# Optimization experiments

Measured on AMD Instinct MI355X. Metric: run time of the kernel, lower is better.

Reference implementation:

```python
import jax, jax.numpy as jnp
import numpy as np

K = 3
PAD = 1


def conv3x3(x, w):
    # x: [B,C,H,W], w: [O,C,3,3] -> [B,O,H,W], stride 1, pad 1, no bias
    return jax.lax.conv_general_dilated(
        x, w, window_strides=(1, 1), padding=((PAD, PAD), (PAD, PAD)),
        dimension_numbers=("NCHW", "OIHW", "NCHW"))


def bilinear_gather(x, py, px):
    """Zero-padded bilinear sampling (torchvision deform_conv2d semantics).
    x: [B,C,H,W]; py, px: [B,KK,H,W] absolute sampling coords.
    Returns [B,C,KK,H,W]."""
    B, C, H, W = x.shape
    KK = py.shape[1]
    y0 = jnp.floor(py)
    x0 = jnp.floor(px)
    wy1 = py - y0  # frac weights
    wx1 = px - x0
    wy0 = 1.0 - wy1
    wx0 = 1.0 - wx1
    x_flat = x.reshape(B, C, H * W)

    def corner(yi, xi, w):
        valid = (yi >= 0) & (yi <= H - 1) & (xi >= 0) & (xi <= W - 1)
        yc = jnp.clip(yi, 0, H - 1).astype(jnp.int32)
        xc = jnp.clip(xi, 0, W - 1).astype(jnp.int32)
        idx = (yc * W + xc).reshape(B, 1, KK * H * W)
        v = jnp.take_along_axis(x_flat, jnp.broadcast_to(idx, (B, C, KK * H * W)), axis=2)
        v = v.reshape(B, C, KK, H, W)
        return v * (w * valid.astype(x.dtype))[:, None]

    return (corner(y0, x0, wy0 * wx0) + corner(y0, x0 + 1.0, wy0 * wx1)
            + corner(y0 + 1.0, x0, wy1 * wx0) + corner(y0 + 1.0, x0 + 1.0, wy1 * wx1))


def deform_conv2d(x, offset, weight):
    """x: [B,C,H,W]; offset: [B,2*K*K,H,W] (dy,dx interleaved per tap, row-major);
    weight: [O,C,K,K]. stride 1, pad 1, dilation 1, 1 group, 1 offset group."""
    B, C, H, W = x.shape
    O = weight.shape[0]
    off = offset.reshape(B, K * K, 2, H, W)
    dy, dx = off[:, :, 0], off[:, :, 1]  # [B,9,H,W]
    ki, kj = jnp.meshgrid(jnp.arange(K, dtype=x.dtype), jnp.arange(K, dtype=x.dtype), indexing="ij")
    ki = ki.reshape(1, K * K, 1, 1)
    kj = kj.reshape(1, K * K, 1, 1)
    hh = jnp.arange(H, dtype=x.dtype).reshape(1, 1, H, 1)
    ww = jnp.arange(W, dtype=x.dtype).reshape(1, 1, 1, W)
    py = hh - PAD + ki + dy  # [B,9,H,W]
    px = ww - PAD + kj + dx
    sampled = bilinear_gather(x, py, px)  # [B,C,9,H,W]
    return jnp.einsum("bckhw,ock->bohw", sampled, weight.reshape(O, C, K * K))


def offset_estimator(x, w1, w2, w3):
    # channel-preserving bottleneck stand-in for Dynamic_offset_estimator
    h = jax.nn.relu(conv3x3(x, w1))
    h = jax.nn.relu(conv3x3(h, w2))
    return conv3x3(h, w3)


def setup_inputs() -> dict:
    key = jax.random.key(0)
    ks = jax.random.split(key, 7)
    B, C, H, W = 1, 768, 64, 64
    C2, CM = 2 * C, 192
    f32 = jnp.float32
    inp = {
        "input_features": jax.random.normal(ks[0], (B, C, H, W), dtype=f32),
        "reference_features": jax.random.normal(ks[1], (B, C, H, W), dtype=f32),
        "est_w1": jax.random.normal(ks[2], (CM, C2, K, K), dtype=f32) / np.sqrt(C2 * K * K),
        "est_w2": jax.random.normal(ks[3], (CM, CM, K, K), dtype=f32) / np.sqrt(CM * K * K),
        "est_w3": jax.random.normal(ks[4], (C2, CM, K, K), dtype=f32) / np.sqrt(CM * K * K),
        "offset_w": jax.random.normal(ks[5], (18, C2, K, K), dtype=f32) / np.sqrt(C2 * K * K),
        "deform_w": jax.random.normal(ks[6], (C, C, K, K), dtype=f32) / np.sqrt(C * K * K),
    }
    return inp


def reference(input_features, reference_features, est_w1, est_w2, est_w3, offset_w, deform_w):
    input_offset = jnp.concatenate([input_features, reference_features], axis=1)  # [B,2C,H,W]
    est = offset_estimator(input_offset, est_w1, est_w2, est_w3)  # [B,2C,H,W]
    offset = conv3x3(est, offset_w)  # [B,18,H,W]
    return deform_conv2d(reference_features, offset, deform_w)  # [B,C,H,W]
```

## Files before the change

kernel.cpp:

```cpp
#include <hip/hip_runtime.h>

#define HWPX 4096

typedef short s8v  __attribute__((ext_vector_type(8)));
typedef float f4v  __attribute__((ext_vector_type(4)));

__device__ inline unsigned short f2bf(float f) {
    unsigned u = __float_as_uint(f);
    return (unsigned short)((u + 0x7fffu + ((u >> 16) & 1u)) >> 16);
}
__device__ inline float bf2f(unsigned s) {
    return __uint_as_float(s << 16);
}

#define GLDS16(gsrc, ldst) \
    __builtin_amdgcn_global_load_lds( \
        (const __attribute__((address_space(1))) unsigned int*)(gsrc), \
        (__attribute__((address_space(3))) unsigned int*)(ldst), 16, 0, 0)

__global__ __launch_bounds__(256)
void tr_cat_k(const float* __restrict__ xa, const float* __restrict__ xb,
              short* __restrict__ xt)
{
    __shared__ __align__(16) short T[64 * 72];
    const int c0 = blockIdx.x * 64, p0 = blockIdx.y * 64, tid = threadIdx.x;
    for (int i = tid; i < 4096; i += 256) {
        int cl = i >> 6, pl = i & 63;
        int c = c0 + cl;
        float v = (c < 768) ? xa[(size_t)c * HWPX + p0 + pl]
                            : xb[(size_t)(c - 768) * HWPX + p0 + pl];
        T[pl * 72 + cl] = (short)f2bf(v);
    }
    __syncthreads();
    for (int i = tid; i < 512; i += 256) {
        int pl = i >> 3, part = i & 7;
        uint4 v = *(const uint4*)&T[pl * 72 + part * 8];
        *(uint4*)&xt[(size_t)(p0 + pl) * 1536 + c0 + part * 8] = v;
    }
}

__device__ inline void wpack1(const float* __restrict__ src, short* __restrict__ dst,
                              int i, int Cin, int Cout, int S, int NB)
{
    int e = i & 7, lane = (i >> 3) & 63;
    int lm = lane & 15, quad = lane >> 4;
    int rest = i >> 9;
    int f = rest % NB;
    int s = (rest / NB) % S;
    int g = rest / (NB * S);
    int cout = g * (NB * 16) + f * 16 + lm;
    int cb = s / 9, t = s % 9;
    int ch = cb * 32 + quad * 8 + e;
    dst[i] = (cout < Cout) ? (short)f2bf(src[((size_t)cout * Cin + ch) * 9 + t]) : 0;
}

#define C1 2654208
#define C2 2985984
#define C3 5640192
#define C4 6082560
#define C5 11390976

__global__ __launch_bounds__(256)
void wpack_all_k(const float* __restrict__ s1, const float* __restrict__ s2,
                 const float* __restrict__ s3, const float* __restrict__ s4,
                 const float* __restrict__ s5,
                 short* __restrict__ d1, short* __restrict__ d2,
                 short* __restrict__ d3, short* __restrict__ d4,
                 short* __restrict__ d5)
{
    int i = blockIdx.x * 256 + threadIdx.x;
    if (i < C1)      wpack1(s1, d1, i,      1536, 192,  432, 4);
    else if (i < C2) wpack1(s2, d2, i - C1, 192,  192,  54,  2);
    else if (i < C3) wpack1(s3, d3, i - C2, 192,  1536, 54,  4);
    else if (i < C4) wpack1(s4, d4, i - C3, 1536, 18,   432, 2);
    else if (i < C5) wpack1(s5, d5, i - C4, 768,  768,  216, 4);
}

template<int NB>
__global__ __launch_bounds__(256, 3)
void convf_k(const short* __restrict__ Xt, int CinStr,
             const short* __restrict__ Wp, int S, int chunks,
             short* __restrict__ Out, int Cstr, int splitStride)
{
    __shared__ __align__(16) short sH[6 * 66 * 40];
    const int tid = threadIdx.x, lane = tid & 63, wv = tid >> 6;
    const int lm = lane & 15, quad = lane >> 4;
    const int r0 = blockIdx.x * 4;
    const int g  = blockIdx.y;
    const int cb0 = blockIdx.z * chunks;
    short* out = Out + (size_t)blockIdx.z * splitStride;

    f4v acc[4][NB];
#pragma unroll
    for (int ma = 0; ma < 4; ++ma)
#pragma unroll
        for (int nb = 0; nb < NB; ++nb)
#pragma unroll
            for (int r = 0; r < 4; ++r) acc[ma][nb][r] = 0.f;

    for (int cc = 0; cc < chunks; ++cc) {
        const int cb = cb0 + cc;
        const short* wpB = Wp + ((size_t)(g * S + cb * 9) * NB) * 512 + lane * 8;
        s8v bb[NB];
#pragma unroll
        for (int f = 0; f < NB; ++f)
            bb[f] = *(const s8v*)&wpB[(size_t)f * 512];

        for (int i = tid; i < 1584; i += 256) {
            int slot = i >> 2, part = i & 3;
            int hr = slot / 66, px = slot % 66;
            int gy = r0 - 1 + hr, gx = px - 1;
            uint4 v = {0, 0, 0, 0};
            if (gy >= 0 && gy < 64 && gx >= 0 && gx < 64)
                v = *(const uint4*)&Xt[(size_t)(gy * 64 + gx) * CinStr + cb * 32 + part * 8];
            *(uint4*)&sH[slot * 40 + part * 8] = v;
        }
        __syncthreads();

#pragma unroll
        for (int t = 0; t < 9; ++t) {
            const int ty = t / 3, tx = t % 3;
            s8v nxt[NB];
#pragma unroll
            for (int f = 0; f < NB; ++f)
                nxt[f] = *(const s8v*)&wpB[(size_t)((t + 1) * NB + f) * 512];
            s8v a[4];
#pragma unroll
            for (int ma = 0; ma < 4; ++ma)
                a[ma] = *(const s8v*)&sH[((wv + ty) * 66 + ma * 16 + lm + tx) * 40 + quad * 8];
#pragma unroll
            for (int ma = 0; ma < 4; ++ma)
#pragma unroll
                for (int nb = 0; nb < NB; ++nb)
                    acc[ma][nb] = __builtin_amdgcn_mfma_f32_16x16x32_bf16(
                        a[ma], bb[nb], acc[ma][nb], 0, 0, 0);
#pragma unroll
            for (int f = 0; f < NB; ++f) bb[f] = nxt[f];
        }
        __syncthreads();
    }

    const int py = (r0 + wv) * 64;
#pragma unroll
    for (int ma = 0; ma < 4; ++ma)
#pragma unroll
        for (int nb = 0; nb < NB; ++nb)
#pragma unroll
            for (int r = 0; r < 4; ++r)
                out[(size_t)(py + ma * 16 + quad * 4 + r) * Cstr
                    + g * (NB * 16) + nb * 16 + lm] = (short)f2bf(acc[ma][nb][r]);
}

__global__ __launch_bounds__(256)
void ep_sumb_k(const short* __restrict__ P, short* __restrict__ outb,
               int nsplit, size_t splitStride, int n8, int relu)
{
    int i = blockIdx.x * 256 + threadIdx.x;
    if (i >= n8) return;
    size_t base = (size_t)i * 8;
    float s[8];
#pragma unroll
    for (int j = 0; j < 8; ++j) s[j] = 0.f;
    for (int sp = 0; sp < nsplit; ++sp) {
        uint4 v = *(const uint4*)&P[sp * splitStride + base];
        s[0] += bf2f(v.x & 0xffffu); s[1] += bf2f(v.x >> 16);
        s[2] += bf2f(v.y & 0xffffu); s[3] += bf2f(v.y >> 16);
        s[4] += bf2f(v.z & 0xffffu); s[5] += bf2f(v.z >> 16);
        s[6] += bf2f(v.w & 0xffffu); s[7] += bf2f(v.w >> 16);
    }
    if (relu) {
#pragma unroll
        for (int j = 0; j < 8; ++j) s[j] = fmaxf(s[j], 0.f);
    }
    uint4 o;
    o.x = f2bf(s[0]) | ((unsigned)f2bf(s[1]) << 16);
    o.y = f2bf(s[2]) | ((unsigned)f2bf(s[3]) << 16);
    o.z = f2bf(s[4]) | ((unsigned)f2bf(s[5]) << 16);
    o.w = f2bf(s[6]) | ((unsigned)f2bf(s[7]) << 16);
    *(uint4*)&outb[base] = o;
}

__global__ __launch_bounds__(256)
void ep_offs_k(const short* __restrict__ P, float* __restrict__ offs, int nsplit)
{
    int i = blockIdx.x * 256 + threadIdx.x;
    if (i >= 18 * HWPX) return;
    int m = i >> 12, px = i & 4095;
    float s = 0.f;
    for (int sp = 0; sp < nsplit; ++sp)
        s += bf2f((unsigned short)P[((size_t)sp * HWPX + px) * 32 + m]);
    offs[i] = s;
}

__global__ __launch_bounds__(256)
void sample_k(const short* __restrict__ xcat, const float* __restrict__ offs,
              short* __restrict__ Smp)
{
    __shared__ int   s_mi[9][16][4];
    __shared__ float s_mw[9][16][4];
    const int tid = threadIdx.x;
    const int p0  = blockIdx.x * 16;
    const int cbq = blockIdx.y * 6;
    const int wv  = tid >> 6, lane = tid & 63;
    const int lmx = lane & 15, qd = lane >> 4;
    const int pg  = p0 >> 6, ma = (p0 >> 4) & 3;

    if (tid < 144) {
        int t = tid / 16, p = tid % 16;
        int pxg = p0 + p;
        int r = pxg >> 6, x = pxg & 63;
        float dy = offs[(size_t)(2 * t)     * HWPX + pxg];
        float dx = offs[(size_t)(2 * t + 1) * HWPX + pxg];
        float py  = (float)(r - 1 + t / 3) + dy;
        float pxf = (float)(x - 1 + t % 3) + dx;
        py  = fminf(fmaxf(py,  -1e6f), 1e6f);
        pxf = fminf(fmaxf(pxf, -1e6f), 1e6f);
        float y0f = floorf(py), x0f = floorf(pxf);
        float wy1 = py - y0f, wx1 = pxf - x0f;
        float wy0 = 1.f - wy1, wx0 = 1.f - wx1;
        bool vy0 = (y0f >=  0.f) && (y0f <= 63.f);
        bool vy1 = (y0f >= -1.f) && (y0f <= 62.f);
        bool vx0 = (x0f >=  0.f) && (x0f <= 63.f);
        bool vx1 = (x0f >= -1.f) && (x0f <= 62.f);
        int y0 = (int)fminf(fmaxf(y0f,       0.f), 63.f);
        int y1 = (int)fminf(fmaxf(y0f + 1.f, 0.f), 63.f);
        int x0 = (int)fminf(fmaxf(x0f,       0.f), 63.f);
        int x1 = (int)fminf(fmaxf(x0f + 1.f, 0.f), 63.f);
        s_mi[t][p][0] = y0 * 64 + x0;  s_mw[t][p][0] = (vy0 && vx0) ? wy0 * wx0 : 0.f;
        s_mi[t][p][1] = y0 * 64 + x1;  s_mw[t][p][1] = (vy0 && vx1) ? wy0 * wx1 : 0.f;
        s_mi[t][p][2] = y1 * 64 + x0;  s_mw[t][p][2] = (vy1 && vx0) ? wy1 * wx0 : 0.f;
        s_mi[t][p][3] = y1 * 64 + x1;  s_mw[t][p][3] = (vy1 && vx1) ? wy1 * wx1 : 0.f;
    }
    __syncthreads();

    for (int j = wv; j < 54; j += 4) {
        const int t = j / 6, cb = cbq + j % 6;
        int   mi[4];
        float mw[4];
#pragma unroll
        for (int c = 0; c < 4; ++c) {
            mi[c] = s_mi[t][lmx][c];
            mw[c] = s_mw[t][lmx][c];
        }
        float a[8];
#pragma unroll
        for (int k = 0; k < 8; ++k) a[k] = 0.f;
#pragma unroll
        for (int c = 0; c < 4; ++c) {
            float wgt = mw[c];
            const short* src = xcat + (size_t)mi[c] * 1536 + 768 + cb * 32 + qd * 8;
            uint4 v = *(const uint4*)src;
            a[0] += wgt * bf2f(v.x & 0xffffu); a[1] += wgt * bf2f(v.x >> 16);
            a[2] += wgt * bf2f(v.y & 0xffffu); a[3] += wgt * bf2f(v.y >> 16);
            a[4] += wgt * bf2f(v.z & 0xffffu); a[5] += wgt * bf2f(v.z >> 16);
            a[6] += wgt * bf2f(v.w & 0xffffu); a[7] += wgt * bf2f(v.w >> 16);
        }
        uint4 o;
        o.x = f2bf(a[0]) | ((unsigned)f2bf(a[1]) << 16);
        o.y = f2bf(a[2]) | ((unsigned)f2bf(a[3]) << 16);
        o.z = f2bf(a[4]) | ((unsigned)f2bf(a[5]) << 16);
        o.w = f2bf(a[6]) | ((unsigned)f2bf(a[7]) << 16);
        size_t addr = ((((size_t)pg * 216 + cb * 9 + t) * 4 + ma) * 64 + lane) * 8;
        *(uint4*)&Smp[addr] = o;
    }
}

__global__ __launch_bounds__(256, 3)
void dgemm_k(const short* __restrict__ Ap, const short* __restrict__ Bp,
             short* __restrict__ P)
{
    __shared__ __align__(16) short sL[3 * 8192];

    const int tid = threadIdx.x, lane = tid & 63, wv = tid >> 6;
    const int lm = lane & 15, quad = lane >> 4;
    const int mg = blockIdx.y * 2 + (wv >> 1);
    const int pg = blockIdx.x * 2 + (wv & 1);
    const int s0 = blockIdx.z * 54;

    const short* stSrc;
    int stChunk;
    if (wv < 2) {
        stSrc = Ap + ((size_t)(blockIdx.y * 2 + wv) * 216 + s0) * 2048;
        stChunk = wv * 2048;
    } else {
        stSrc = Bp + ((size_t)(blockIdx.x * 2 + (wv - 2)) * 216 + s0) * 2048;
        stChunk = 4096 + (wv - 2) * 2048;
    }

    f4v acc[4][4];
#pragma unroll
    for (int ma = 0; ma < 4; ++ma)
#pragma unroll
        for (int nb = 0; nb < 4; ++nb)
#pragma unroll
            for (int r = 0; r < 4; ++r) acc[ma][nb][r] = 0.f;

#pragma unroll
    for (int j = 0; j < 4; ++j)
        GLDS16(stSrc + (size_t)0 * 2048 + j * 512 + lane * 8,
               &sL[0 * 8192 + stChunk + j * 512]);
#pragma unroll
    for (int j = 0; j < 4; ++j)
        GLDS16(stSrc + (size_t)1 * 2048 + j * 512 + lane * 8,
               &sL[1 * 8192 + stChunk + j * 512]);
    asm volatile("s_waitcnt vmcnt(4)" ::: "memory");
    __builtin_amdgcn_s_barrier();
    __builtin_amdgcn_sched_barrier(0);

    const int aOff = (wv >> 1) * 2048;
    const int bOff = 4096 + (wv & 1) * 2048;

    s8v avA[4], bvA[4], avB[4], bvB[4];
#pragma unroll
    for (int f = 0; f < 4; ++f) {
        avA[f] = *(const s8v*)&sL[0 * 8192 + aOff + f * 512 + lane * 8];
        bvA[f] = *(const s8v*)&sL[0 * 8192 + bOff + f * 512 + lane * 8];
    }

    int cA = 0, cB = 1, cC = 2;

    for (int s = 0; s < 52; s += 2) {
#pragma unroll
        for (int j = 0; j < 4; ++j)
            GLDS16(stSrc + (size_t)(s + 2) * 2048 + j * 512 + lane * 8,
                   &sL[cC * 8192 + stChunk + j * 512]);
        asm volatile("s_waitcnt vmcnt(4)" ::: "memory");
        __builtin_amdgcn_s_barrier();
        __builtin_amdgcn_sched_barrier(0);
        {
            const int base = cB * 8192;
#pragma unroll
            for (int f = 0; f < 4; ++f) {
                avB[f] = *(const s8v*)&sL[base + aOff + f * 512 + lane * 8];
                bvB[f] = *(const s8v*)&sL[base + bOff + f * 512 + lane * 8];
            }
        }
#pragma unroll
        for (int ma = 0; ma < 4; ++ma)
#pragma unroll
            for (int nb = 0; nb < 4; ++nb)
                acc[ma][nb] = __builtin_amdgcn_mfma_f32_16x16x32_bf16(
                    avA[ma], bvA[nb], acc[ma][nb], 0, 0, 0);

#pragma unroll
        for (int j = 0; j < 4; ++j)
            GLDS16(stSrc + (size_t)(s + 3) * 2048 + j * 512 + lane * 8,
                   &sL[cA * 8192 + stChunk + j * 512]);
        asm volatile("s_waitcnt vmcnt(4)" ::: "memory");
        __builtin_amdgcn_s_barrier();
        __builtin_amdgcn_sched_barrier(0);
        {
            const int base = cC * 8192;
#pragma unroll
            for (int f = 0; f < 4; ++f) {
                avA[f] = *(const s8v*)&sL[base + aOff + f * 512 + lane * 8];
                bvA[f] = *(const s8v*)&sL[base + bOff + f * 512 + lane * 8];
            }
        }
#pragma unroll
        for (int ma = 0; ma < 4; ++ma)
#pragma unroll
            for (int nb = 0; nb < 4; ++nb)
                acc[ma][nb] = __builtin_amdgcn_mfma_f32_16x16x32_bf16(
                    avB[ma], bvB[nb], acc[ma][nb], 0, 0, 0);

        int nA = cC, nB = cA, nC = cB;
        cA = nA; cB = nB; cC = nC;
    }

    asm volatile("s_waitcnt vmcnt(0)" ::: "memory");
    __builtin_amdgcn_s_barrier();
    __builtin_amdgcn_sched_barrier(0);
    {
        const int base = cB * 8192;
#pragma unroll
        for (int f = 0; f < 4; ++f) {
            avB[f] = *(const s8v*)&sL[base + aOff + f * 512 + lane * 8];
            bvB[f] = *(const s8v*)&sL[base + bOff + f * 512 + lane * 8];
        }
    }
#pragma unroll
    for (int ma = 0; ma < 4; ++ma)
#pragma unroll
        for (int nb = 0; nb < 4; ++nb)
            acc[ma][nb] = __builtin_amdgcn_mfma_f32_16x16x32_bf16(
                avA[ma], bvA[nb], acc[ma][nb], 0, 0, 0);
#pragma unroll
    for (int ma = 0; ma < 4; ++ma)
#pragma unroll
        for (int nb = 0; nb < 4; ++nb)
            acc[ma][nb] = __builtin_amdgcn_mfma_f32_16x16x32_bf16(
                avB[ma], bvB[nb], acc[ma][nb], 0, 0, 0);

    short* p = P + (size_t)blockIdx.z * 768 * HWPX;
#pragma unroll
    for (int ma = 0; ma < 4; ++ma)
#pragma unroll
        for (int nb = 0; nb < 4; ++nb)
#pragma unroll
            for (int r = 0; r < 4; ++r)
                p[(size_t)(mg * 64 + ma * 16 + quad * 4 + r) * HWPX
                  + pg * 64 + nb * 16 + lm] = (short)f2bf(acc[ma][nb][r]);
}

__global__ __launch_bounds__(256)
void ep_dg_k(const short* __restrict__ P, float* __restrict__ out)
{
    int i = blockIdx.x * 256 + threadIdx.x;
    if (i >= 768 * HWPX / 8) return;
    size_t base = (size_t)i * 8;
    float s[8];
#pragma unroll
    for (int j = 0; j < 8; ++j) s[j] = 0.f;
    for (int sp = 0; sp < 4; ++sp) {
        uint4 v = *(const uint4*)&P[(size_t)sp * 768 * HWPX + base];
        s[0] += bf2f(v.x & 0xffffu); s[1] += bf2f(v.x >> 16);
        s[2] += bf2f(v.y & 0xffffu); s[3] += bf2f(v.y >> 16);
        s[4] += bf2f(v.z & 0xffffu); s[5] += bf2f(v.z >> 16);
        s[6] += bf2f(v.w & 0xffffu); s[7] += bf2f(v.w >> 16);
    }
    float4 o0 = make_float4(s[0], s[1], s[2], s[3]);
    float4 o1 = make_float4(s[4], s[5], s[6], s[7]);
    *(float4*)&out[base]     = o0;
    *(float4*)&out[base + 4] = o1;
}

extern "C" void kernel_launch(void* const* d_in, const int* in_sizes, int n_in,
                              void* d_out, int out_size, void* d_ws, size_t ws_size,
                              hipStream_t stream)
{
    const float* x_in  = (const float*)d_in[0];
    const float* x_ref = (const float*)d_in[1];
    const float* w1    = (const float*)d_in[2];
    const float* w2    = (const float*)d_in[3];
    const float* w3    = (const float*)d_in[4];
    const float* ow    = (const float*)d_in[5];
    const float* dw    = (const float*)d_in[6];
    float* out = (float*)d_out;

    char* w = (char*)d_ws;
    size_t off = 0;
    auto carve = [&](size_t bytes) {
        void* p = w + off;
        off += (bytes + 255) & ~(size_t)255;
        return p;
    };
    short* xcat = (short*)carve((size_t)4096 * 1536 * 2);
    short* w1p  = (short*)carve((size_t)C1 * 2);
    short* w2p  = (short*)carve((size_t)(C2 - C1) * 2);
    short* w3p  = (short*)carve((size_t)(C3 - C2) * 2);
    short* w4p  = (short*)carve((size_t)(C4 - C3) * 2);
    short* dwp  = (short*)carve((size_t)(C5 - C4) * 2);
    float* offs = (float*)carve((size_t)18 * 4096 * 4);
    short* Smp  = (short*)carve((size_t)4096 * 6912 * 2);
    char*  R    = (char*)carve((size_t)2 * 768 * 4096 * 4);
    short* rh1  = (short*)R;
    short* rh2  = (short*)(R + 1572864);
    short* est  = (short*)(R + 3145728);
    short* Pcv  = Smp;
    short* Pdg  = (short*)R;

    tr_cat_k<<<dim3(24, 64), 256, 0, stream>>>(x_in, x_ref, xcat);
    wpack_all_k<<<(C5 + 255) / 256, 256, 0, stream>>>(w1, w2, w3, ow, dw,
                                                      w1p, w2p, w3p, w4p, dwp);

    const int n8 = 4096 * 192 / 8;
    convf_k<4><<<dim3(16, 3, 16), 256, 0, stream>>>(xcat, 1536, w1p, 432, 3,
                                                    Pcv, 192, 4096 * 192);
    ep_sumb_k<<<(n8 + 255) / 256, 256, 0, stream>>>(Pcv, rh1, 16, (size_t)4096 * 192, n8, 1);
    convf_k<2><<<dim3(16, 6, 6), 256, 0, stream>>>(rh1, 192, w2p, 54, 1,
                                                   Pcv, 192, 4096 * 192);
    ep_sumb_k<<<(n8 + 255) / 256, 256, 0, stream>>>(Pcv, rh2, 6, (size_t)4096 * 192, n8, 1);
    convf_k<4><<<dim3(16, 24, 2), 256, 0, stream>>>(rh2, 192, w3p, 54, 3,
                                                    Pcv, 1536, 4096 * 1536);
    {
        const int n8c3 = 4096 * 1536 / 8;
        ep_sumb_k<<<(n8c3 + 255) / 256, 256, 0, stream>>>(Pcv, est, 2, (size_t)4096 * 1536, n8c3, 0);
    }
    convf_k<2><<<dim3(16, 1, 48), 256, 0, stream>>>(est, 1536, w4p, 432, 1,
                                                    Pcv, 32, 4096 * 32);
    ep_offs_k<<<(18 * HWPX + 255) / 256, 256, 0, stream>>>(Pcv, offs, 48);
    sample_k<<<dim3(256, 4), 256, 0, stream>>>(xcat, offs, Smp);
    dgemm_k<<<dim3(32, 6, 4), 256, 0, stream>>>(dwp, Smp, Pdg);
    ep_dg_k<<<(768 * HWPX / 8 + 255) / 256, 256, 0, stream>>>(Pdg, out);
}
```

Baseline: 329.8 us.

## Fuse split-K partial sum into offset conv loads and merge prep kernels

The two split-K partial outputs of the third estimator conv are now summed on the fly while the fourth conv loads its input tile, so the separate ep_sumb reduction kernel and the round trip through the est buffer go away. The transpose/concat kernel and the weight-pack kernel are merged into one launch that picks its role from the block index. The cost is that the offset conv now reads two bf16 buffers and redoes the add-and-round for every halo load, and each value is loaded about three times because of halo overlap. Offset partials now go to a separate p4 buffer so they do not overwrite the Pcv inputs that are still being read.

```diff
diff --git a/kernel.cpp b/kernel.cpp
--- a/kernel.cpp
+++ b/kernel.cpp
@@ -18,26 +18,11 @@
         (const __attribute__((address_space(1))) unsigned int*)(gsrc), \
         (__attribute__((address_space(3))) unsigned int*)(ldst), 16, 0, 0)
 
-__global__ __launch_bounds__(256)
-void tr_cat_k(const float* __restrict__ xa, const float* __restrict__ xb,
-              short* __restrict__ xt)
-{
-    __shared__ __align__(16) short T[64 * 72];
-    const int c0 = blockIdx.x * 64, p0 = blockIdx.y * 64, tid = threadIdx.x;
-    for (int i = tid; i < 4096; i += 256) {
-        int cl = i >> 6, pl = i & 63;
-        int c = c0 + cl;
-        float v = (c < 768) ? xa[(size_t)c * HWPX + p0 + pl]
-                            : xb[(size_t)(c - 768) * HWPX + p0 + pl];
-        T[pl * 72 + cl] = (short)f2bf(v);
-    }
-    __syncthreads();
-    for (int i = tid; i < 512; i += 256) {
-        int pl = i >> 3, part = i & 7;
-        uint4 v = *(const uint4*)&T[pl * 72 + part * 8];
-        *(uint4*)&xt[(size_t)(p0 + pl) * 1536 + c0 + part * 8] = v;
-    }
-}
+#define C1 2654208
+#define C2 2985984
+#define C3 5640192
+#define C4 6082560
+#define C5 11390976
 
 __device__ inline void wpack1(const float* __restrict__ src, short* __restrict__ dst,
                               int i, int Cin, int Cout, int S, int NB)
@@ -54,31 +39,48 @@
     dst[i] = (cout < Cout) ? (short)f2bf(src[((size_t)cout * Cin + ch) * 9 + t]) : 0;
 }
 
-#define C1 2654208
-#define C2 2985984
-#define C3 5640192
-#define C4 6082560
-#define C5 11390976
-
 __global__ __launch_bounds__(256)
-void wpack_all_k(const float* __restrict__ s1, const float* __restrict__ s2,
-                 const float* __restrict__ s3, const float* __restrict__ s4,
-                 const float* __restrict__ s5,
-                 short* __restrict__ d1, short* __restrict__ d2,
-                 short* __restrict__ d3, short* __restrict__ d4,
-                 short* __restrict__ d5)
-{
-    int i = blockIdx.x * 256 + threadIdx.x;
-    if (i < C1)      wpack1(s1, d1, i,      1536, 192,  432, 4);
-    else if (i < C2) wpack1(s2, d2, i - C1, 192,  192,  54,  2);
-    else if (i < C3) wpack1(s3, d3, i - C2, 192,  1536, 54,  4);
-    else if (i < C4) wpack1(s4, d4, i - C3, 1536, 18,   432, 2);
-    else if (i < C5) wpack1(s5, d5, i - C4, 768,  768,  216, 4);
-}
-
-template<int NB>
+void prep_k(const float* __restrict__ xa, const float* __restrict__ xb,
+            short* __restrict__ xt,
+            const float* __restrict__ s1, const float* __restrict__ s2,
+            const float* __restrict__ s3, const float* __restrict__ s4,
+            const float* __restrict__ s5,
+            short* __restrict__ d1, short* __restrict__ d2,
+            short* __restrict__ d3, short* __restrict__ d4,
+            short* __restrict__ d5)
+{
+    __shared__ __align__(16) short T[64 * 72];
+    const int tid = threadIdx.x;
+    if (blockIdx.x < 1536) {
+        const int b = blockIdx.x;
+        const int c0 = (b % 24) * 64, p0 = (b / 24) * 64;
+        for (int i = tid; i < 4096; i += 256) {
+            int cl = i >> 6, pl = i & 63;
+            int c = c0 + cl;
+            float v = (c < 768) ? xa[(size_t)c * HWPX + p0 + pl]
+                                : xb[(size_t)(c - 768) * HWPX + p0 + pl];
+            T[pl * 72 + cl] = (short)f2bf(v);
+        }
+        __syncthreads();
+        for (int i = tid; i < 512; i += 256) {
+            int pl = i >> 3, part = i & 7;
+            uint4 v = *(const uint4*)&T[pl * 72 + part * 8];
+            *(uint4*)&xt[(size_t)(p0 + pl) * 1536 + c0 + part * 8] = v;
+        }
+    } else {
+        int i = (blockIdx.x - 1536) * 256 + tid;
+        if (i < C1)      wpack1(s1, d1, i,      1536, 192,  432, 4);
+        else if (i < C2) wpack1(s2, d2, i - C1, 192,  192,  54,  2);
+        else if (i < C3) wpack1(s3, d3, i - C2, 192,  1536, 54,  4);
+        else if (i < C4) wpack1(s4, d4, i - C3, 1536, 18,   432, 2);
+        else if (i < C5) wpack1(s5, d5, i - C4, 768,  768,  216, 4);
+    }
+}
+
+template<int NB, bool SUM2>
 __global__ __launch_bounds__(256, 3)
-void convf_k(const short* __restrict__ Xt, int CinStr,
+void convf_k(const short* __restrict__ Xt, const short* __restrict__ Xt2,
+             int CinStr,
              const short* __restrict__ Wp, int S, int chunks,
              short* __restrict__ Out, int Cstr, int splitStride)
 {
@@ -111,8 +113,21 @@
             int hr = slot / 66, px = slot % 66;
             int gy = r0 - 1 + hr, gx = px - 1;
             uint4 v = {0, 0, 0, 0};
-            if (gy >= 0 && gy < 64 && gx >= 0 && gx < 64)
-                v = *(const uint4*)&Xt[(size_t)(gy * 64 + gx) * CinStr + cb * 32 + part * 8];
+            if (gy >= 0 && gy < 64 && gx >= 0 && gx < 64) {
+                size_t base = (size_t)(gy * 64 + gx) * CinStr + cb * 32 + part * 8;
+                v = *(const uint4*)&Xt[base];
+                if (SUM2) {
+                    uint4 v2 = *(const uint4*)&Xt2[base];
+                    unsigned* a = (unsigned*)&v;
+                    const unsigned* b = (const unsigned*)&v2;
+#pragma unroll
+                    for (int k = 0; k < 4; ++k) {
+                        float lo = bf2f(a[k] & 0xffffu) + bf2f(b[k] & 0xffffu);
+                        float hi = bf2f(a[k] >> 16)     + bf2f(b[k] >> 16);
+                        a[k] = f2bf(lo) | ((unsigned)f2bf(hi) << 16);
+                    }
+                }
+            }
             *(uint4*)&sH[slot * 40 + part * 8] = v;
         }
         __syncthreads();
@@ -456,30 +471,25 @@
     char*  R    = (char*)carve((size_t)2 * 768 * 4096 * 4);
     short* rh1  = (short*)R;
     short* rh2  = (short*)(R + 1572864);
-    short* est  = (short*)(R + 3145728);
+    short* p4   = (short*)(R + 3145728);
     short* Pcv  = Smp;
     short* Pdg  = (short*)R;
 
-    tr_cat_k<<<dim3(24, 64), 256, 0, stream>>>(x_in, x_ref, xcat);
-    wpack_all_k<<<(C5 + 255) / 256, 256, 0, stream>>>(w1, w2, w3, ow, dw,
-                                                      w1p, w2p, w3p, w4p, dwp);
+    prep_k<<<1536 + (C5 + 255) / 256, 256, 0, stream>>>(
+        x_in, x_ref, xcat, w1, w2, w3, ow, dw, w1p, w2p, w3p, w4p, dwp);
 
     const int n8 = 4096 * 192 / 8;
-    convf_k<4><<<dim3(16, 3, 16), 256, 0, stream>>>(xcat, 1536, w1p, 432, 3,
-                                                    Pcv, 192, 4096 * 192);
+    convf_k<4, false><<<dim3(16, 3, 16), 256, 0, stream>>>(
+        xcat, nullptr, 1536, w1p, 432, 3, Pcv, 192, 4096 * 192);
     ep_sumb_k<<<(n8 + 255) / 256, 256, 0, stream>>>(Pcv, rh1, 16, (size_t)4096 * 192, n8, 1);
-    convf_k<2><<<dim3(16, 6, 6), 256, 0, stream>>>(rh1, 192, w2p, 54, 1,
-                                                   Pcv, 192, 4096 * 192);
+    convf_k<2, false><<<dim3(16, 6, 6), 256, 0, stream>>>(
+        rh1, nullptr, 192, w2p, 54, 1, Pcv, 192, 4096 * 192);
     ep_sumb_k<<<(n8 + 255) / 256, 256, 0, stream>>>(Pcv, rh2, 6, (size_t)4096 * 192, n8, 1);
-    convf_k<4><<<dim3(16, 24, 2), 256, 0, stream>>>(rh2, 192, w3p, 54, 3,
-                                                    Pcv, 1536, 4096 * 1536);
-    {
-        const int n8c3 = 4096 * 1536 / 8;
-        ep_sumb_k<<<(n8c3 + 255) / 256, 256, 0, stream>>>(Pcv, est, 2, (size_t)4096 * 1536, n8c3, 0);
-    }
-    convf_k<2><<<dim3(16, 1, 48), 256, 0, stream>>>(est, 1536, w4p, 432, 1,
-                                                    Pcv, 32, 4096 * 32);
-    ep_offs_k<<<(18 * HWPX + 255) / 256, 256, 0, stream>>>(Pcv, offs, 48);
+    convf_k<4, false><<<dim3(16, 24, 2), 256, 0, stream>>>(
+        rh2, nullptr, 192, w3p, 54, 3, Pcv, 1536, 4096 * 1536);
+    convf_k<2, true><<<dim3(16, 1, 48), 256, 0, stream>>>(
+        Pcv, Pcv + (size_t)4096 * 1536, 1536, w4p, 432, 1, p4, 32, 4096 * 32);
+    ep_offs_k<<<(18 * HWPX + 255) / 256, 256, 0, stream>>>(p4, offs, 48);
     sample_k<<<dim3(256, 4), 256, 0, stream>>>(xcat, offs, Smp);
     dgemm_k<<<dim3(32, 6, 4), 256, 0, stream>>>(dwp, Smp, Pdg);
     ep_dg_k<<<(768 * HWPX / 8 + 255) / 256, 256, 0, stream>>>(Pdg, out);
```

Result: faster. 319.9 us (-3.0%).
